# Kernel optimization log

Measured on AMD Instinct MI355X. Metric: run time of the kernel, lower is better.

The kernel has to match this reference:

```python
import jax, jax.numpy as jnp
import numpy as np

E = 1024      # hidden_size
H = 16        # num_attention_heads
HD = E // H   # head_dim
EPS = 1e-5


def _mw_linear(x, Wt, bt, Wi, bi, split):
    # multiway linear: text weights on tokens [:split], image weights on [split:]
    xt = x[:, :split] @ Wt.T + bt
    xi = x[:, split:] @ Wi.T + bi
    return jnp.concatenate([xt, xi], axis=1)


def _ln(x, g, b):
    mu = jnp.mean(x, axis=-1, keepdims=True)
    var = jnp.mean(jnp.square(x - mu), axis=-1, keepdims=True)
    return (x - mu) * jax.lax.rsqrt(var + EPS) * g + b


def _mw_ln(x, gt, bt, gi, bi, split):
    return jnp.concatenate([_ln(x[:, :split], gt, bt), _ln(x[:, split:], gi, bi)], axis=1)


def setup_inputs() -> dict:
    key = jax.random.key(0)
    ks = jax.random.split(key, 24)
    B, T = 8, 1024
    d = {
        'query': jax.random.normal(ks[0], (B, T, E), jnp.float32),
        'key': jax.random.normal(ks[1], (B, T, E), jnp.float32),
        'value': jax.random.normal(ks[2], (B, T, E), jnp.float32),
        'attention_mask': jax.random.normal(ks[3], (T, T), jnp.float32) * 0.02,
    }
    i = 4
    for name in ['q', 'k', 'v', 'o']:
        d[f'W{name}_t'] = jax.random.normal(ks[i], (E, E), jnp.float32) * 0.02; i += 1
        d[f'b{name}_t'] = jnp.zeros((E,), jnp.float32)
        d[f'W{name}_i'] = jax.random.normal(ks[i], (E, E), jnp.float32) * 0.02; i += 1
        d[f'b{name}_i'] = jnp.zeros((E,), jnp.float32)
    d['ln_g_t'] = jnp.ones((E,), jnp.float32)
    d['ln_b_t'] = jnp.zeros((E,), jnp.float32)
    d['ln_g_i'] = jnp.ones((E,), jnp.float32)
    d['ln_b_i'] = jnp.zeros((E,), jnp.float32)
    d['split_position'] = 64
    return d


def reference(query, key, value, attention_mask,
              Wq_t, bq_t, Wq_i, bq_i,
              Wk_t, bk_t, Wk_i, bk_i,
              Wv_t, bv_t, Wv_i, bv_i,
              Wo_t, bo_t, Wo_i, bo_i,
              ln_g_t, ln_b_t, ln_g_i, ln_b_i,
              split_position):
    B, T, _ = query.shape
    S = key.shape[1]
    scaling = HD ** -0.5
    q = _mw_linear(query, Wq_t, bq_t, Wq_i, bq_i, split_position) * scaling
    k = _mw_linear(key, Wk_t, bk_t, Wk_i, bk_i, split_position)
    v = _mw_linear(value, Wv_t, bv_t, Wv_i, bv_i, split_position)
    q = q.reshape(B, T, H, HD)
    k = k.reshape(B, S, H, HD)
    v = v.reshape(B, S, H, HD)
    # [B, H, T, S] attention logits
    attn_weights = jnp.einsum('bthd,bshd->bhts', q, k)
    attn_weights = jnp.nan_to_num(attn_weights) + attention_mask[None, None]
    probs = jax.nn.softmax(attn_weights.astype(jnp.float32), axis=-1).astype(attn_weights.dtype)
    attn = jnp.einsum('bhts,bshd->bthd', probs, v).reshape(B, T, E)
    attn = _mw_ln(attn, ln_g_t, ln_b_t, ln_g_i, ln_b_i, split_position)
    attn = _mw_linear(attn, Wo_t, bo_t, Wo_i, bo_i, split_position)
    return attn
```

## Files before the change

### kernel.cpp

```cpp
#include <hip/hip_runtime.h>

#define E_DIM 1024
#define HEADS 16
#define HD 64

typedef unsigned short ushort_t;
typedef __attribute__((ext_vector_type(8))) short bf16x8;
typedef __attribute__((ext_vector_type(4))) float floatx4;

__device__ inline unsigned int pack2bf(float a, float b) {
    unsigned int ua = __builtin_bit_cast(unsigned int, a);
    unsigned int ub = __builtin_bit_cast(unsigned int, b);
    ua = (ua + 0x8000u) >> 16;
    ub = (ub + 0x8000u) & 0xFFFF0000u;
    return ua | ub;
}
__device__ inline unsigned short f2bf(float a) {
    return (unsigned short)((__builtin_bit_cast(unsigned int, a) + 0x8000u) >> 16);
}
__device__ inline float bf2f(unsigned int s) {
    return __builtin_bit_cast(float, s << 16);
}

__device__ __forceinline__ void load_lds16(const void* g, void* l) {
    __builtin_amdgcn_global_load_lds(
        (const __attribute__((address_space(1))) unsigned int*)g,
        (__attribute__((address_space(3))) unsigned int*)l, 16, 0, 0);
}

__global__ __launch_bounds__(256) void cvt_inputs(
    const float* s0, const float* s1, const float* s2,
    ushort_t* d0, ushort_t* d1, ushort_t* d2)
{
    const float* __restrict__ src = (blockIdx.y == 0) ? s0 : (blockIdx.y == 1) ? s1 : s2;
    ushort_t* __restrict__ dst = (blockIdx.y == 0) ? d0 : (blockIdx.y == 1) ? d1 : d2;
    size_t i = ((size_t)blockIdx.x * 256 + threadIdx.x) * 8;
    float4 a = *(const float4*)&src[i];
    float4 b = *(const float4*)&src[i + 4];
    uint4 o;
    o.x = pack2bf(a.x, a.y); o.y = pack2bf(a.z, a.w);
    o.z = pack2bf(b.x, b.y); o.w = pack2bf(b.z, b.w);
    *(uint4*)&dst[i] = o;
}

__global__ __launch_bounds__(256) void cvt_weights(
    const float* w0, const float* w1, const float* w2, const float* w3,
    const float* w4, const float* w5, const float* w6, const float* w7,
    ushort_t* __restrict__ out)
{
    const float* srcs[8] = {w0, w1, w2, w3, w4, w5, w6, w7};
    const float* __restrict__ src = srcs[blockIdx.y];
    ushort_t* __restrict__ dst = out + (size_t)blockIdx.y * E_DIM * E_DIM;
    size_t i = ((size_t)blockIdx.x * 256 + threadIdx.x) * 8;
    float4 a = *(const float4*)&src[i];
    float4 b = *(const float4*)&src[i + 4];
    uint4 o;
    o.x = pack2bf(a.x, a.y); o.y = pack2bf(a.z, a.w);
    o.z = pack2bf(b.x, b.y); o.w = pack2bf(b.z, b.w);
    *(uint4*)&dst[i] = o;
}

template<bool OUT_BF16>
__device__ __forceinline__ void gemm_core(
    const ushort_t* __restrict__ x, const ushort_t* __restrict__ W,
    const float* __restrict__ bias, void* __restrict__ outv,
    int m0, int n0, int split, int kind, float scale, int T_)
{
    __shared__ __align__(16) ushort_t As[128 * 32];
    __shared__ __align__(16) ushort_t Bs[128 * 32];

    const int tid  = threadIdx.x;
    const int lane = tid & 63;
    const int wv   = tid >> 6;
    const int rw   = (wv >> 1) * 64;
    const int cw   = (wv & 1) * 64;
    const int am   = lane & 15;
    const int aq   = lane >> 4;

    const int grow = wv * 32 + (lane >> 2);
    const int gcol = (lane & 3) * 8;

    floatx4 acc[4][4];
    #pragma unroll
    for (int i = 0; i < 4; ++i)
        #pragma unroll
        for (int j = 0; j < 4; ++j)
            acc[i][j] = (floatx4){0.f, 0.f, 0.f, 0.f};

    for (int k0 = 0; k0 < E_DIM; k0 += 32) {
        load_lds16(&x[(size_t)(m0 + grow) * E_DIM + k0 + gcol],      &As[(wv * 32) * 32]);
        load_lds16(&x[(size_t)(m0 + grow + 16) * E_DIM + k0 + gcol], &As[(wv * 32 + 16) * 32]);
        load_lds16(&W[(size_t)(n0 + grow) * E_DIM + k0 + gcol],      &Bs[(wv * 32) * 32]);
        load_lds16(&W[(size_t)(n0 + grow + 16) * E_DIM + k0 + gcol], &Bs[(wv * 32 + 16) * 32]);
        __syncthreads();

        bf16x8 af[4], bfv[4];
        #pragma unroll
        for (int i = 0; i < 4; ++i)
            af[i] = *(const bf16x8*)&As[(rw + i * 16 + am) * 32 + aq * 8];
        #pragma unroll
        for (int j = 0; j < 4; ++j)
            bfv[j] = *(const bf16x8*)&Bs[(cw + j * 16 + am) * 32 + aq * 8];

        #pragma unroll
        for (int i = 0; i < 4; ++i)
            #pragma unroll
            for (int j = 0; j < 4; ++j)
                acc[i][j] = __builtin_amdgcn_mfma_f32_16x16x32_bf16(af[i], bfv[j], acc[i][j], 0, 0, 0);
        __syncthreads();
    }

    const int cq = lane >> 4;
    const int cm = lane & 15;
    #pragma unroll
    for (int j = 0; j < 4; ++j) {
        int n = n0 + cw + j * 16 + cm;
        float bv = bias[n];
        #pragma unroll
        for (int i = 0; i < 4; ++i) {
            int mbase = m0 + rw + i * 16 + cq * 4;
            #pragma unroll
            for (int r = 0; r < 4; ++r) {
                int m = mbase + r;
                int t = m % T_;
                if (((t < split) ? 0 : 1) != kind) continue;
                float val = (acc[i][j][r] + bv) * scale;
                if (OUT_BF16) ((ushort_t*)outv)[(size_t)m * E_DIM + n] = f2bf(val);
                else          ((float*)outv)[(size_t)m * E_DIM + n] = val;
            }
        }
    }
}

__global__ __launch_bounds__(256) void gemm_qkv(
    const ushort_t* __restrict__ xq, const ushort_t* __restrict__ xk,
    const ushort_t* __restrict__ xv, const ushort_t* __restrict__ wall,
    const float* bq_t, const float* bq_i, const float* bk_t, const float* bk_i,
    const float* bv_t, const float* bv_i,
    ushort_t* oq, ushort_t* ok, ushort_t* ov,
    const int* __restrict__ split_ptr, int T_)
{
    const int split = *split_ptr;
    const int z = blockIdx.z;
    const int op = z >> 1;
    const int kind = z & 1;
    const int m0 = blockIdx.y * 128;
    const int n0 = blockIdx.x * 128;
    const int t0 = m0 % T_;

    if (kind == 0) { if (t0 >= split) return; }
    else           { if (t0 + 128 <= split) return; }

    const ushort_t* x = (op == 0) ? xq : (op == 1) ? xk : xv;
    ushort_t* outp    = (op == 0) ? oq : (op == 1) ? ok : ov;
    const ushort_t* W = wall + (size_t)z * E_DIM * E_DIM;
    const float* bias = (op == 0) ? (kind ? bq_i : bq_t)
                      : (op == 1) ? (kind ? bk_i : bk_t)
                                  : (kind ? bv_i : bv_t);
    float scale = (op == 0) ? 0.125f : 1.0f;

    gemm_core<true>(x, W, bias, outp, m0, n0, split, kind, scale, T_);
}

__global__ __launch_bounds__(256) void gemm_o(
    const ushort_t* __restrict__ x, const ushort_t* __restrict__ Wt,
    const float* bt, const ushort_t* __restrict__ Wi, const float* bi,
    float* __restrict__ outp, const int* __restrict__ split_ptr, int T_)
{
    const int split = *split_ptr;
    const int kind = blockIdx.z;
    const int m0 = blockIdx.y * 128;
    const int n0 = blockIdx.x * 128;
    const int t0 = m0 % T_;

    if (kind == 0) { if (t0 >= split) return; }
    else           { if (t0 + 128 <= split) return; }

    gemm_core<false>(x, kind ? Wi : Wt, kind ? bi : bt, outp, m0, n0, split, kind, 1.0f, T_);
}

__global__ __launch_bounds__(256) void attn_mfma4(
    const ushort_t* __restrict__ q, const ushort_t* __restrict__ k,
    const ushort_t* __restrict__ v, const float* __restrict__ mask,
    ushort_t* __restrict__ outp, int T_)
{
    const int tid  = threadIdx.x;
    const int lane = tid & 63;
    const int wv   = tid >> 6;
    const int b    = blockIdx.x;
    const int h    = blockIdx.y;
    const int r0   = blockIdx.z * 128;

    __shared__ __align__(16) unsigned short Ks[5120];
    __shared__ __align__(16) unsigned short Vst[5120];
    __shared__ __align__(16) unsigned short Ps[4 * 1280];

    const int m    = lane & 15;
    const int kq   = lane >> 4;
    const int wrow = wv * 16;

    bf16x8 aq[2][2];
    #pragma unroll
    for (int qs = 0; qs < 2; ++qs)
        #pragma unroll
        for (int c = 0; c < 2; ++c)
            aq[qs][c] = *(const bf16x8*)&q[((size_t)(b * T_ + r0 + qs * 64 + wrow + m)) * E_DIM
                                           + h * HD + c * 32 + kq * 8];

    floatx4 oa[2][4];
    float mrun[2][4], lsum[2][4];
    #pragma unroll
    for (int qs = 0; qs < 2; ++qs)
        #pragma unroll
        for (int j = 0; j < 4; ++j) {
            oa[qs][j] = (floatx4){0.f, 0.f, 0.f, 0.f};
            mrun[qs][j] = -3.0e38f; lsum[qs][j] = 0.f;
        }

    const int krow = tid >> 4;
    const int kc4  = (tid & 15) * 4;
    const int kad  = (kc4 >> 5) * 2560 + krow * 40 + (kc4 & 31);
    const int vs0  = (tid >> 4) * 4;
    const int vd0  = (tid & 15) * 4;
    const int vplane = (vs0 >> 5) * 2560;
    const int vsin   = vs0 & 31;

    uint2 kreg[4], vreg[4];

    #pragma unroll
    for (int i = 0; i < 4; ++i)
        kreg[i] = *(const uint2*)&k[((size_t)(b * T_ + krow + 16 * i)) * E_DIM + h * HD + kc4];
    #pragma unroll
    for (int i = 0; i < 4; ++i)
        vreg[i] = *(const uint2*)&v[((size_t)(b * T_ + vs0 + i)) * E_DIM + h * HD + vd0];

    #pragma unroll
    for (int i = 0; i < 4; ++i) {
        int ad = kad + 16 * i * 40;
        *(unsigned int*)&Ks[ad]     = kreg[i].x;
        *(unsigned int*)&Ks[ad + 2] = kreg[i].y;
    }
    {
        const ushort_t* vp = (const ushort_t*)vreg;
        #pragma unroll
        for (int t = 0; t < 4; ++t) {
            int d  = vd0 + t;
            int pr = d ^ ((d >> 4) & 3);
            uint2 w;
            w.x = (unsigned int)vp[0 * 4 + t] | ((unsigned int)vp[1 * 4 + t] << 16);
            w.y = (unsigned int)vp[2 * 4 + t] | ((unsigned int)vp[3 * 4 + t] << 16);
            *(uint2*)&Vst[vplane + pr * 40 + vsin] = w;
        }
    }
    __syncthreads();

    const int NT = T_ / 64;
    #pragma unroll 1
    for (int it = 0; it < NT; ++it) {
        const int s0 = it * 64;

        if (it + 1 < NT) {
            int s0n = s0 + 64;
            #pragma unroll
            for (int i = 0; i < 4; ++i)
                kreg[i] = *(const uint2*)&k[((size_t)(b * T_ + s0n + krow + 16 * i)) * E_DIM + h * HD + kc4];
            #pragma unroll
            for (int i = 0; i < 4; ++i)
                vreg[i] = *(const uint2*)&v[((size_t)(b * T_ + s0n + vs0 + i)) * E_DIM + h * HD + vd0];
        }

        #pragma unroll
        for (int qs = 0; qs < 2; ++qs) {
            float mv[4][4];
            {
                const float* mbase = &mask[(size_t)(r0 + qs * 64 + wrow + kq * 4) * T_ + s0 + m];
                #pragma unroll
                for (int j = 0; j < 4; ++j)
                    #pragma unroll
                    for (int r = 0; r < 4; ++r)
                        mv[j][r] = mbase[r * T_ + j * 16];
            }

            floatx4 sa[4];
            #pragma unroll
            for (int j = 0; j < 4; ++j) sa[j] = (floatx4){0.f, 0.f, 0.f, 0.f};
            __builtin_amdgcn_s_setprio(1);
            #pragma unroll
            for (int c = 0; c < 2; ++c) {
                #pragma unroll
                for (int j = 0; j < 4; ++j) {
                    bf16x8 bk = *(const bf16x8*)&Ks[c * 2560 + (j * 16 + m) * 40 + kq * 8];
                    sa[j] = __builtin_amdgcn_mfma_f32_16x16x32_bf16(aq[qs][c], bk, sa[j], 0, 0, 0);
                }
            }
            __builtin_amdgcn_s_setprio(0);

            float mt[4];
            #pragma unroll
            for (int r = 0; r < 4; ++r) {
                sa[0][r] += mv[0][r]; sa[1][r] += mv[1][r];
                sa[2][r] += mv[2][r]; sa[3][r] += mv[3][r];
                float m2 = fmaxf(fmaxf(sa[0][r], sa[1][r]), fmaxf(sa[2][r], sa[3][r]));
                m2 = fmaxf(m2, __shfl_xor(m2, 1));
                m2 = fmaxf(m2, __shfl_xor(m2, 2));
                m2 = fmaxf(m2, __shfl_xor(m2, 4));
                m2 = fmaxf(m2, __shfl_xor(m2, 8));
                mt[r] = m2;
            }
            float need = fmaxf(fmaxf(mt[0] - mrun[qs][0], mt[1] - mrun[qs][1]),
                               fmaxf(mt[2] - mrun[qs][2], mt[3] - mrun[qs][3]));
            if (!__all(need <= 8.0f)) {
                #pragma unroll
                for (int r = 0; r < 4; ++r) {
                    float mn = fmaxf(mrun[qs][r], mt[r]);
                    float a  = __expf(mrun[qs][r] - mn);
                    mrun[qs][r] = mn;
                    lsum[qs][r] *= a;
                    #pragma unroll
                    for (int j = 0; j < 4; ++j)
                        oa[qs][j][r] *= a;
                }
            }

            float rs[4] = {0.f, 0.f, 0.f, 0.f};
            #pragma unroll
            for (int j = 0; j < 4; ++j) {
                int gl = ((((j & 1) << 1) | (m >> 3)) ^ kq) & 3;
                int pbase = wv * 1280 + (j >> 1) * 640 + (kq * 4) * 40 + gl * 8 + (m & 7);
                #pragma unroll
                for (int r = 0; r < 4; ++r) {
                    float p = __expf(sa[j][r] - mrun[qs][r]);
                    rs[r] += p;
                    Ps[pbase + r * 40] = f2bf(p);
                }
            }
            #pragma unroll
            for (int r = 0; r < 4; ++r) {
                float s = rs[r];
                s += __shfl_xor(s, 1); s += __shfl_xor(s, 2);
                s += __shfl_xor(s, 4); s += __shfl_xor(s, 8);
                lsum[qs][r] += s;
            }

            __builtin_amdgcn_s_setprio(1);
            #pragma unroll
            for (int c = 0; c < 2; ++c) {
                bf16x8 ap = *(const bf16x8*)&Ps[wv * 1280 + c * 640 + m * 40 + ((kq ^ (m >> 2)) & 3) * 8];
                #pragma unroll
                for (int j = 0; j < 4; ++j) {
                    int pr = 16 * j + (m ^ j);
                    bf16x8 bv = *(const bf16x8*)&Vst[c * 2560 + pr * 40 + kq * 8];
                    oa[qs][j] = __builtin_amdgcn_mfma_f32_16x16x32_bf16(ap, bv, oa[qs][j], 0, 0, 0);
                }
            }
            __builtin_amdgcn_s_setprio(0);
        }

        if (it + 1 < NT) {
            __syncthreads();
            #pragma unroll
            for (int i = 0; i < 4; ++i) {
                int ad = kad + 16 * i * 40;
                *(unsigned int*)&Ks[ad]     = kreg[i].x;
                *(unsigned int*)&Ks[ad + 2] = kreg[i].y;
            }
            const ushort_t* vp = (const ushort_t*)vreg;
            #pragma unroll
            for (int t = 0; t < 4; ++t) {
                int d  = vd0 + t;
                int pr = d ^ ((d >> 4) & 3);
                uint2 w;
                w.x = (unsigned int)vp[0 * 4 + t] | ((unsigned int)vp[1 * 4 + t] << 16);
                w.y = (unsigned int)vp[2 * 4 + t] | ((unsigned int)vp[3 * 4 + t] << 16);
                *(uint2*)&Vst[vplane + pr * 40 + vsin] = w;
            }
            __syncthreads();
        }
    }

    #pragma unroll
    for (int qs = 0; qs < 2; ++qs)
        #pragma unroll
        for (int r = 0; r < 4; ++r) {
            float inv = 1.0f / lsum[qs][r];
            size_t orow = ((size_t)(b * T_ + r0 + qs * 64 + wrow + kq * 4 + r)) * E_DIM + h * HD;
            #pragma unroll
            for (int j = 0; j < 4; ++j)
                outp[orow + j * 16 + m] = f2bf(oa[qs][j][r] * inv);
        }
}

__global__ __launch_bounds__(256) void mw_ln_bf16(
    const ushort_t* __restrict__ x,
    const float* __restrict__ gt, const float* __restrict__ bt,
    const float* __restrict__ gi, const float* __restrict__ bi,
    ushort_t* __restrict__ out,
    const int* __restrict__ split_ptr, int T_)
{
    const int split = *split_ptr;
    const int row = blockIdx.x;
    const int t = row % T_;
    const float* __restrict__ g  = (t < split) ? gt : gi;
    const float* __restrict__ bb = (t < split) ? bt : bi;

    const int tid = threadIdx.x;
    const int lane = tid & 63;
    const int wid = tid >> 6;

    __shared__ float red[8];

    uint2 xv = *(const uint2*)&x[(size_t)row * E_DIM + tid * 4];
    float f0 = bf2f(xv.x & 0xffffu), f1 = bf2f(xv.x >> 16);
    float f2 = bf2f(xv.y & 0xffffu), f3 = bf2f(xv.y >> 16);
    float s = f0 + f1 + f2 + f3;
    #pragma unroll
    for (int off = 1; off < 64; off <<= 1) s += __shfl_xor(s, off, 64);
    if (lane == 0) red[wid] = s;
    __syncthreads();
    float mu = (red[0] + red[1] + red[2] + red[3]) * (1.0f / E_DIM);

    float d0 = f0 - mu, d1 = f1 - mu, d2 = f2 - mu, d3 = f3 - mu;
    float s2 = d0*d0 + d1*d1 + d2*d2 + d3*d3;
    #pragma unroll
    for (int off = 1; off < 64; off <<= 1) s2 += __shfl_xor(s2, off, 64);
    if (lane == 0) red[4 + wid] = s2;
    __syncthreads();
    float var = (red[4] + red[5] + red[6] + red[7]) * (1.0f / E_DIM);
    float rstd = rsqrtf(var + 1e-5f);

    float4 gv = *(const float4*)&g[tid * 4];
    float4 bv = *(const float4*)&bb[tid * 4];
    uint2 ov;
    ov.x = pack2bf(d0 * rstd * gv.x + bv.x, d1 * rstd * gv.y + bv.y);
    ov.y = pack2bf(d2 * rstd * gv.z + bv.z, d3 * rstd * gv.w + bv.w);
    *(uint2*)&out[(size_t)row * E_DIM + tid * 4] = ov;
}

extern "C" void kernel_launch(void* const* d_in, const int* in_sizes, int n_in,
                              void* d_out, int out_size, void* d_ws, size_t ws_size,
                              hipStream_t stream) {
    const float* query = (const float*)d_in[0];
    const float* key   = (const float*)d_in[1];
    const float* value = (const float*)d_in[2];
    const float* mask  = (const float*)d_in[3];
    const float* Wq_t = (const float*)d_in[4];  const float* bq_t = (const float*)d_in[5];
    const float* Wq_i = (const float*)d_in[6];  const float* bq_i = (const float*)d_in[7];
    const float* Wk_t = (const float*)d_in[8];  const float* bk_t = (const float*)d_in[9];
    const float* Wk_i = (const float*)d_in[10]; const float* bk_i = (const float*)d_in[11];
    const float* Wv_t = (const float*)d_in[12]; const float* bv_t = (const float*)d_in[13];
    const float* Wv_i = (const float*)d_in[14]; const float* bv_i = (const float*)d_in[15];
    const float* Wo_t = (const float*)d_in[16]; const float* bo_t = (const float*)d_in[17];
    const float* Wo_i = (const float*)d_in[18]; const float* bo_i = (const float*)d_in[19];
    const float* ln_g_t = (const float*)d_in[20]; const float* ln_b_t = (const float*)d_in[21];
    const float* ln_g_i = (const float*)d_in[22]; const float* ln_b_i = (const float*)d_in[23];
    const int* split = (const int*)d_in[24];

    float* out = (float*)d_out;

    const int BT = in_sizes[0] / E_DIM;
    const int T_ = 1024;
    const int B  = BT / T_;

    ushort_t* ws = (ushort_t*)d_ws;
    const size_t nx = (size_t)BT * E_DIM;
    const size_t nw = (size_t)E_DIM * E_DIM;
    ushort_t* xq_bf = ws;
    ushort_t* xk_bf = ws + nx;
    ushort_t* xv_bf = ws + 2 * nx;
    ushort_t* k_bf  = ws + 3 * nx;
    ushort_t* v_bf  = ws + 4 * nx;
    ushort_t* w_bf  = ws + 5 * nx;
    ushort_t* q_bf  = (ushort_t*)d_out;

    dim3 blk(256);
    const int cvt_blocks = (int)(nx / 2048);
    const int wcvt_blocks = (int)(nw / 2048);

    cvt_weights<<<dim3(wcvt_blocks, 8), blk, 0, stream>>>(
        Wq_t, Wq_i, Wk_t, Wk_i, Wv_t, Wv_i, Wo_t, Wo_i, w_bf);
    cvt_inputs<<<dim3(cvt_blocks, 3), blk, 0, stream>>>(
        query, key, value, xq_bf, xk_bf, xv_bf);

    gemm_qkv<<<dim3(E_DIM / 128, BT / 128, 6), blk, 0, stream>>>(
        xq_bf, xk_bf, xv_bf, w_bf,
        bq_t, bq_i, bk_t, bk_i, bv_t, bv_i,
        q_bf, k_bf, v_bf, split, T_);

    attn_mfma4<<<dim3(B, HEADS, T_ / 128), blk, 0, stream>>>(
        q_bf, k_bf, v_bf, mask, q_bf, T_);

    mw_ln_bf16<<<dim3(BT), blk, 0, stream>>>(
        q_bf, ln_g_t, ln_b_t, ln_g_i, ln_b_i, xq_bf, split, T_);

    gemm_o<<<dim3(E_DIM / 128, BT / 128, 2), blk, 0, stream>>>(
        xq_bf, w_bf + 6 * nw, bo_t, w_bf + 7 * nw, bo_i, out, split, T_);
}
```

Before: 498.2 us.

## Share K/V LDS fragments across both query sub-tiles and defer row-sum reduction

Restructures the attention inner loop so the QK^T MFMAs for both 64-row query sub-tiles run together, each K fragment read from LDS once and reused for both. The PV stage likewise loads V fragments once and applies them to both sub-tiles, which needs a doubled P buffer in LDS. Per-row softmax sums are kept per-lane and shuffle-reduced only once at the end instead of every iteration. This cuts LDS reads and shuffles but raises register pressure (two score accumulators live) and LDS footprint, which could lower occupancy.

Result: faster. 478.9 us (-3.9%).

```diff
diff --git a/kernel.cpp b/kernel.cpp
--- a/kernel.cpp
+++ b/kernel.cpp
@@ -193,7 +193,7 @@
 
     __shared__ __align__(16) unsigned short Ks[5120];
     __shared__ __align__(16) unsigned short Vst[5120];
-    __shared__ __align__(16) unsigned short Ps[4 * 1280];
+    __shared__ __align__(16) unsigned short Ps[8 * 1280];
 
     const int m    = lane & 15;
     const int kq   = lane >> 4;
@@ -268,6 +268,26 @@
             for (int i = 0; i < 4; ++i)
                 vreg[i] = *(const uint2*)&v[((size_t)(b * T_ + s0n + vs0 + i)) * E_DIM + h * HD + vd0];
         }
+
+        floatx4 sa[2][4];
+        #pragma unroll
+        for (int qs = 0; qs < 2; ++qs)
+            #pragma unroll
+            for (int j = 0; j < 4; ++j) sa[qs][j] = (floatx4){0.f, 0.f, 0.f, 0.f};
+        __builtin_amdgcn_s_setprio(1);
+        #pragma unroll
+        for (int c = 0; c < 2; ++c) {
+            bf16x8 bkf[4];
+            #pragma unroll
+            for (int j = 0; j < 4; ++j)
+                bkf[j] = *(const bf16x8*)&Ks[c * 2560 + (j * 16 + m) * 40 + kq * 8];
+            #pragma unroll
+            for (int qs = 0; qs < 2; ++qs)
+                #pragma unroll
+                for (int j = 0; j < 4; ++j)
+                    sa[qs][j] = __builtin_amdgcn_mfma_f32_16x16x32_bf16(aq[qs][c], bkf[j], sa[qs][j], 0, 0, 0);
+        }
+        __builtin_amdgcn_s_setprio(0);
 
         #pragma unroll
         for (int qs = 0; qs < 2; ++qs) {
@@ -281,26 +301,13 @@
                         mv[j][r] = mbase[r * T_ + j * 16];
             }
 
-            floatx4 sa[4];
-            #pragma unroll
-            for (int j = 0; j < 4; ++j) sa[j] = (floatx4){0.f, 0.f, 0.f, 0.f};
-            __builtin_amdgcn_s_setprio(1);
-            #pragma unroll
-            for (int c = 0; c < 2; ++c) {
-                #pragma unroll
-                for (int j = 0; j < 4; ++j) {
-                    bf16x8 bk = *(const bf16x8*)&Ks[c * 2560 + (j * 16 + m) * 40 + kq * 8];
-                    sa[j] = __builtin_amdgcn_mfma_f32_16x16x32_bf16(aq[qs][c], bk, sa[j], 0, 0, 0);
-                }
-            }
-            __builtin_amdgcn_s_setprio(0);
-
             float mt[4];
             #pragma unroll
             for (int r = 0; r < 4; ++r) {
-                sa[0][r] += mv[0][r]; sa[1][r] += mv[1][r];
-                sa[2][r] += mv[2][r]; sa[3][r] += mv[3][r];
-                float m2 = fmaxf(fmaxf(sa[0][r], sa[1][r]), fmaxf(sa[2][r], sa[3][r]));
+                sa[qs][0][r] += mv[0][r]; sa[qs][1][r] += mv[1][r];
+                sa[qs][2][r] += mv[2][r]; sa[qs][3][r] += mv[3][r];
+                float m2 = fmaxf(fmaxf(sa[qs][0][r], sa[qs][1][r]),
+                                 fmaxf(sa[qs][2][r], sa[qs][3][r]));
                 m2 = fmaxf(m2, __shfl_xor(m2, 1));
                 m2 = fmaxf(m2, __shfl_xor(m2, 2));
                 m2 = fmaxf(m2, __shfl_xor(m2, 4));
@@ -322,39 +329,38 @@
                 }
             }
 
-            float rs[4] = {0.f, 0.f, 0.f, 0.f};
             #pragma unroll
             for (int j = 0; j < 4; ++j) {
                 int gl = ((((j & 1) << 1) | (m >> 3)) ^ kq) & 3;
-                int pbase = wv * 1280 + (j >> 1) * 640 + (kq * 4) * 40 + gl * 8 + (m & 7);
+                int pbase = (wv * 2 + qs) * 1280 + (j >> 1) * 640 + (kq * 4) * 40 + gl * 8 + (m & 7);
                 #pragma unroll
                 for (int r = 0; r < 4; ++r) {
-                    float p = __expf(sa[j][r] - mrun[qs][r]);
-                    rs[r] += p;
+                    float p = __expf(sa[qs][j][r] - mrun[qs][r]);
+                    lsum[qs][r] += p;
                     Ps[pbase + r * 40] = f2bf(p);
                 }
             }
-            #pragma unroll
-            for (int r = 0; r < 4; ++r) {
-                float s = rs[r];
-                s += __shfl_xor(s, 1); s += __shfl_xor(s, 2);
-                s += __shfl_xor(s, 4); s += __shfl_xor(s, 8);
-                lsum[qs][r] += s;
-            }
-
-            __builtin_amdgcn_s_setprio(1);
-            #pragma unroll
-            for (int c = 0; c < 2; ++c) {
-                bf16x8 ap = *(const bf16x8*)&Ps[wv * 1280 + c * 640 + m * 40 + ((kq ^ (m >> 2)) & 3) * 8];
+        }
+
+        __builtin_amdgcn_s_setprio(1);
+        #pragma unroll
+        for (int c = 0; c < 2; ++c) {
+            bf16x8 bvf[4];
+            #pragma unroll
+            for (int j = 0; j < 4; ++j) {
+                int pr = 16 * j + (m ^ j);
+                bvf[j] = *(const bf16x8*)&Vst[c * 2560 + pr * 40 + kq * 8];
+            }
+            #pragma unroll
+            for (int qs = 0; qs < 2; ++qs) {
+                bf16x8 ap = *(const bf16x8*)&Ps[(wv * 2 + qs) * 1280 + c * 640 + m * 40
+                                                + ((kq ^ (m >> 2)) & 3) * 8];
                 #pragma unroll
-                for (int j = 0; j < 4; ++j) {
-                    int pr = 16 * j + (m ^ j);
-                    bf16x8 bv = *(const bf16x8*)&Vst[c * 2560 + pr * 40 + kq * 8];
-                    oa[qs][j] = __builtin_amdgcn_mfma_f32_16x16x32_bf16(ap, bv, oa[qs][j], 0, 0, 0);
-                }
-            }
-            __builtin_amdgcn_s_setprio(0);
-        }
+                for (int j = 0; j < 4; ++j)
+                    oa[qs][j] = __builtin_amdgcn_mfma_f32_16x16x32_bf16(ap, bvf[j], oa[qs][j], 0, 0, 0);
+            }
+        }
+        __builtin_amdgcn_s_setprio(0);
 
         if (it + 1 < NT) {
             __syncthreads();
@@ -382,7 +388,10 @@
     for (int qs = 0; qs < 2; ++qs)
         #pragma unroll
         for (int r = 0; r < 4; ++r) {
-            float inv = 1.0f / lsum[qs][r];
+            float s = lsum[qs][r];
+            s += __shfl_xor(s, 1); s += __shfl_xor(s, 2);
+            s += __shfl_xor(s, 4); s += __shfl_xor(s, 8);
+            float inv = 1.0f / s;
             size_t orow = ((size_t)(b * T_ + r0 + qs * 64 + wrow + kq * 4 + r)) * E_DIM + h * HD;
             #pragma unroll
             for (int j = 0; j < 4; ++j)
```

## Rewrite attention with 32x32 MFMA, transposed S^T scores, and exp2 softmax

Applied to the files above, without the earlier changes.

The attention kernel moves from 16x16x32 MFMA tiles to 32x32x16 tiles and computes S^T = K·Q^T, so each lane owns one query row. The P fragments for the PV MFMA are then built in registers with cross-half shuffles instead of a round trip through LDS. The softmax switches to exp2 by folding log2e into the Q scale, and a new pre-pass kernel transposes and pre-scales the mask, written into a freed workspace buffer. The aim is fewer LDS round trips, fewer instructions per tile and cheaper exponentials. In exchange it adds an extra kernel launch, per-element shuffles for the rescale and output steps, and strided mask reads.

After: 488.7 us. About the same (-1.9%).

```diff
diff --git a/kernel.cpp b/kernel.cpp
--- a/kernel.cpp
+++ b/kernel.cpp
@@ -3,10 +3,12 @@
 #define E_DIM 1024
 #define HEADS 16
 #define HD 64
+#define LOG2E 1.44269504088896340736f
 
 typedef unsigned short ushort_t;
 typedef __attribute__((ext_vector_type(8))) short bf16x8;
 typedef __attribute__((ext_vector_type(4))) float floatx4;
+typedef __attribute__((ext_vector_type(16))) float floatx16;
 
 __device__ inline unsigned int pack2bf(float a, float b) {
     unsigned int ua = __builtin_bit_cast(unsigned int, a);
@@ -60,6 +62,32 @@
     *(uint4*)&dst[i] = o;
 }
 
+__global__ __launch_bounds__(256) void mask_tr(
+    const float* __restrict__ m, float* __restrict__ mt, int T_)
+{
+    __shared__ float tile[64][65];
+    const int bx = blockIdx.x * 64;
+    const int by = blockIdx.y * 64;
+    const int tc = (threadIdx.x & 15) * 4;
+    const int tr = threadIdx.x >> 4;
+    #pragma unroll
+    for (int rr = 0; rr < 64; rr += 16) {
+        float4 vv = *(const float4*)&m[(size_t)(by + tr + rr) * T_ + bx + tc];
+        tile[tr + rr][tc]     = vv.x; tile[tr + rr][tc + 1] = vv.y;
+        tile[tr + rr][tc + 2] = vv.z; tile[tr + rr][tc + 3] = vv.w;
+    }
+    __syncthreads();
+    #pragma unroll
+    for (int rr = 0; rr < 64; rr += 16) {
+        float4 ov;
+        ov.x = tile[tc + 0][tr + rr] * LOG2E;
+        ov.y = tile[tc + 1][tr + rr] * LOG2E;
+        ov.z = tile[tc + 2][tr + rr] * LOG2E;
+        ov.w = tile[tc + 3][tr + rr] * LOG2E;
+        *(float4*)&mt[(size_t)(bx + tr + rr) * T_ + by + tc] = ov;
+    }
+}
+
 template<bool OUT_BF16>
 __device__ __forceinline__ void gemm_core(
     const ushort_t* __restrict__ x, const ushort_t* __restrict__ W,
@@ -157,7 +185,7 @@
     const float* bias = (op == 0) ? (kind ? bq_i : bq_t)
                       : (op == 1) ? (kind ? bk_i : bk_t)
                                   : (kind ? bv_i : bv_t);
-    float scale = (op == 0) ? 0.125f : 1.0f;
+    float scale = (op == 0) ? 0.125f * LOG2E : 1.0f;
 
     gemm_core<true>(x, W, bias, outp, m0, n0, split, kind, scale, T_);
 }
@@ -179,9 +207,9 @@
     gemm_core<false>(x, kind ? Wi : Wt, kind ? bi : bt, outp, m0, n0, split, kind, 1.0f, T_);
 }
 
-__global__ __launch_bounds__(256) void attn_mfma4(
+__global__ __launch_bounds__(256) void attn_mfma32(
     const ushort_t* __restrict__ q, const ushort_t* __restrict__ k,
-    const ushort_t* __restrict__ v, const float* __restrict__ mask,
+    const ushort_t* __restrict__ v, const float* __restrict__ maskT,
     ushort_t* __restrict__ outp, int T_)
 {
     const int tid  = threadIdx.x;
@@ -191,65 +219,50 @@
     const int h    = blockIdx.y;
     const int r0   = blockIdx.z * 128;
 
-    __shared__ __align__(16) unsigned short Ks[5120];
-    __shared__ __align__(16) unsigned short Vst[5120];
-    __shared__ __align__(16) unsigned short Ps[4 * 1280];
-
-    const int m    = lane & 15;
-    const int kq   = lane >> 4;
-    const int wrow = wv * 16;
-
-    bf16x8 aq[2][2];
-    #pragma unroll
-    for (int qs = 0; qs < 2; ++qs)
-        #pragma unroll
-        for (int c = 0; c < 2; ++c)
-            aq[qs][c] = *(const bf16x8*)&q[((size_t)(b * T_ + r0 + qs * 64 + wrow + m)) * E_DIM
-                                           + h * HD + c * 32 + kq * 8];
-
-    floatx4 oa[2][4];
-    float mrun[2][4], lsum[2][4];
-    #pragma unroll
-    for (int qs = 0; qs < 2; ++qs)
-        #pragma unroll
-        for (int j = 0; j < 4; ++j) {
-            oa[qs][j] = (floatx4){0.f, 0.f, 0.f, 0.f};
-            mrun[qs][j] = -3.0e38f; lsum[qs][j] = 0.f;
-        }
-
-    const int krow = tid >> 4;
-    const int kc4  = (tid & 15) * 4;
-    const int kad  = (kc4 >> 5) * 2560 + krow * 40 + (kc4 & 31);
-    const int vs0  = (tid >> 4) * 4;
-    const int vd0  = (tid & 15) * 4;
-    const int vplane = (vs0 >> 5) * 2560;
-    const int vsin   = vs0 & 31;
-
-    uint2 kreg[4], vreg[4];
-
+    const int q32 = lane & 31;
+    const int hi  = lane >> 5;
+
+    __shared__ __align__(16) ushort_t Ks[64 * 72];
+    __shared__ __align__(16) ushort_t VT[64 * 72];
+
+    const int qrow = r0 + wv * 32 + q32;
+
+    bf16x8 aqf[4];
+    #pragma unroll
+    for (int dc = 0; dc < 4; ++dc)
+        aqf[dc] = *(const bf16x8*)&q[((size_t)(b * T_ + qrow)) * E_DIM + h * HD + dc * 16 + hi * 8];
+
+    floatx16 oa[2];
+    #pragma unroll
+    for (int n = 0; n < 2; ++n)
+        #pragma unroll
+        for (int i = 0; i < 16; ++i) oa[n][i] = 0.f;
+    float mrun = -1.0e30f, lsum = 0.f;
+
+    const int kr = tid >> 2;
+    const int kc = (tid & 3) * 16;
+    const int vr = (tid >> 4) * 4;
+    const int vc = (tid & 15) * 4;
+
+    uint4 kreg[2];
+    uint2 vreg[4];
+
+    kreg[0] = *(const uint4*)&k[((size_t)(b * T_ + kr)) * E_DIM + h * HD + kc];
+    kreg[1] = *(const uint4*)&k[((size_t)(b * T_ + kr)) * E_DIM + h * HD + kc + 8];
     #pragma unroll
     for (int i = 0; i < 4; ++i)
-        kreg[i] = *(const uint2*)&k[((size_t)(b * T_ + krow + 16 * i)) * E_DIM + h * HD + kc4];
-    #pragma unroll
-    for (int i = 0; i < 4; ++i)
-        vreg[i] = *(const uint2*)&v[((size_t)(b * T_ + vs0 + i)) * E_DIM + h * HD + vd0];
-
-    #pragma unroll
-    for (int i = 0; i < 4; ++i) {
-        int ad = kad + 16 * i * 40;
-        *(unsigned int*)&Ks[ad]     = kreg[i].x;
-        *(unsigned int*)&Ks[ad + 2] = kreg[i].y;
-    }
+        vreg[i] = *(const uint2*)&v[((size_t)(b * T_ + vr + i)) * E_DIM + h * HD + vc];
+
+    *(uint4*)&Ks[kr * 72 + kc]     = kreg[0];
+    *(uint4*)&Ks[kr * 72 + kc + 8] = kreg[1];
     {
         const ushort_t* vp = (const ushort_t*)vreg;
         #pragma unroll
         for (int t = 0; t < 4; ++t) {
-            int d  = vd0 + t;
-            int pr = d ^ ((d >> 4) & 3);
             uint2 w;
             w.x = (unsigned int)vp[0 * 4 + t] | ((unsigned int)vp[1 * 4 + t] << 16);
             w.y = (unsigned int)vp[2 * 4 + t] | ((unsigned int)vp[3 * 4 + t] << 16);
-            *(uint2*)&Vst[vplane + pr * 40 + vsin] = w;
+            *(uint2*)&VT[(vc + t) * 72 + vr] = w;
         }
     }
     __syncthreads();
@@ -260,134 +273,137 @@
         const int s0 = it * 64;
 
         if (it + 1 < NT) {
-            int s0n = s0 + 64;
+            const int sn = s0 + 64;
+            kreg[0] = *(const uint4*)&k[((size_t)(b * T_ + sn + kr)) * E_DIM + h * HD + kc];
+            kreg[1] = *(const uint4*)&k[((size_t)(b * T_ + sn + kr)) * E_DIM + h * HD + kc + 8];
             #pragma unroll
             for (int i = 0; i < 4; ++i)
-                kreg[i] = *(const uint2*)&k[((size_t)(b * T_ + s0n + krow + 16 * i)) * E_DIM + h * HD + kc4];
-            #pragma unroll
-            for (int i = 0; i < 4; ++i)
-                vreg[i] = *(const uint2*)&v[((size_t)(b * T_ + s0n + vs0 + i)) * E_DIM + h * HD + vd0];
+                vreg[i] = *(const uint2*)&v[((size_t)(b * T_ + sn + vr + i)) * E_DIM + h * HD + vc];
         }
 
-        #pragma unroll
-        for (int qs = 0; qs < 2; ++qs) {
-            float mv[4][4];
-            {
-                const float* mbase = &mask[(size_t)(r0 + qs * 64 + wrow + kq * 4) * T_ + s0 + m];
-                #pragma unroll
-                for (int j = 0; j < 4; ++j)
-                    #pragma unroll
-                    for (int r = 0; r < 4; ++r)
-                        mv[j][r] = mbase[r * T_ + j * 16];
-            }
-
-            floatx4 sa[4];
-            #pragma unroll
-            for (int j = 0; j < 4; ++j) sa[j] = (floatx4){0.f, 0.f, 0.f, 0.f};
-            __builtin_amdgcn_s_setprio(1);
-            #pragma unroll
-            for (int c = 0; c < 2; ++c) {
-                #pragma unroll
-                for (int j = 0; j < 4; ++j) {
-                    bf16x8 bk = *(const bf16x8*)&Ks[c * 2560 + (j * 16 + m) * 40 + kq * 8];
-                    sa[j] = __builtin_amdgcn_mfma_f32_16x16x32_bf16(aq[qs][c], bk, sa[j], 0, 0, 0);
-                }
-            }
-            __builtin_amdgcn_s_setprio(0);
-
-            float mt[4];
-            #pragma unroll
-            for (int r = 0; r < 4; ++r) {
-                sa[0][r] += mv[0][r]; sa[1][r] += mv[1][r];
-                sa[2][r] += mv[2][r]; sa[3][r] += mv[3][r];
-                float m2 = fmaxf(fmaxf(sa[0][r], sa[1][r]), fmaxf(sa[2][r], sa[3][r]));
-                m2 = fmaxf(m2, __shfl_xor(m2, 1));
-                m2 = fmaxf(m2, __shfl_xor(m2, 2));
-                m2 = fmaxf(m2, __shfl_xor(m2, 4));
-                m2 = fmaxf(m2, __shfl_xor(m2, 8));
-                mt[r] = m2;
-            }
-            float need = fmaxf(fmaxf(mt[0] - mrun[qs][0], mt[1] - mrun[qs][1]),
-                               fmaxf(mt[2] - mrun[qs][2], mt[3] - mrun[qs][3]));
-            if (!__all(need <= 8.0f)) {
-                #pragma unroll
-                for (int r = 0; r < 4; ++r) {
-                    float mn = fmaxf(mrun[qs][r], mt[r]);
-                    float a  = __expf(mrun[qs][r] - mn);
-                    mrun[qs][r] = mn;
-                    lsum[qs][r] *= a;
-                    #pragma unroll
-                    for (int j = 0; j < 4; ++j)
-                        oa[qs][j][r] *= a;
-                }
-            }
-
-            float rs[4] = {0.f, 0.f, 0.f, 0.f};
-            #pragma unroll
-            for (int j = 0; j < 4; ++j) {
-                int gl = ((((j & 1) << 1) | (m >> 3)) ^ kq) & 3;
-                int pbase = wv * 1280 + (j >> 1) * 640 + (kq * 4) * 40 + gl * 8 + (m & 7);
-                #pragma unroll
-                for (int r = 0; r < 4; ++r) {
-                    float p = __expf(sa[j][r] - mrun[qs][r]);
-                    rs[r] += p;
-                    Ps[pbase + r * 40] = f2bf(p);
-                }
-            }
-            #pragma unroll
-            for (int r = 0; r < 4; ++r) {
-                float s = rs[r];
-                s += __shfl_xor(s, 1); s += __shfl_xor(s, 2);
-                s += __shfl_xor(s, 4); s += __shfl_xor(s, 8);
-                lsum[qs][r] += s;
-            }
-
-            __builtin_amdgcn_s_setprio(1);
-            #pragma unroll
-            for (int c = 0; c < 2; ++c) {
-                bf16x8 ap = *(const bf16x8*)&Ps[wv * 1280 + c * 640 + m * 40 + ((kq ^ (m >> 2)) & 3) * 8];
-                #pragma unroll
-                for (int j = 0; j < 4; ++j) {
-                    int pr = 16 * j + (m ^ j);
-                    bf16x8 bv = *(const bf16x8*)&Vst[c * 2560 + pr * 40 + kq * 8];
-                    oa[qs][j] = __builtin_amdgcn_mfma_f32_16x16x32_bf16(ap, bv, oa[qs][j], 0, 0, 0);
-                }
-            }
-            __builtin_amdgcn_s_setprio(0);
+        float mv[2][16];
+        #pragma unroll
+        for (int j = 0; j < 2; ++j)
+            #pragma unroll
+            for (int i = 0; i < 16; ++i) {
+                int sr = s0 + 32 * j + (i & 3) + 8 * (i >> 2) + 4 * hi;
+                mv[j][i] = maskT[(size_t)sr * T_ + qrow];
+            }
+
+        floatx16 sa[2];
+        #pragma unroll
+        for (int j = 0; j < 2; ++j)
+            #pragma unroll
+            for (int i = 0; i < 16; ++i) sa[j][i] = 0.f;
+        __builtin_amdgcn_s_setprio(1);
+        #pragma unroll
+        for (int j = 0; j < 2; ++j)
+            #pragma unroll
+            for (int dc = 0; dc < 4; ++dc) {
+                bf16x8 kf = *(const bf16x8*)&Ks[(32 * j + q32) * 72 + dc * 16 + hi * 8];
+                sa[j] = __builtin_amdgcn_mfma_f32_32x32x16_bf16(kf, aqf[dc], sa[j], 0, 0, 0);
+            }
+        __builtin_amdgcn_s_setprio(0);
+
+        #pragma unroll
+        for (int j = 0; j < 2; ++j)
+            #pragma unroll
+            for (int i = 0; i < 16; ++i) sa[j][i] += mv[j][i];
+
+        float mx8[8];
+        #pragma unroll
+        for (int u = 0; u < 8; ++u)
+            mx8[u] = fmaxf(fmaxf(sa[0][2 * u], sa[0][2 * u + 1]),
+                           fmaxf(sa[1][2 * u], sa[1][2 * u + 1]));
+        float mt = fmaxf(fmaxf(fmaxf(mx8[0], mx8[1]), fmaxf(mx8[2], mx8[3])),
+                         fmaxf(fmaxf(mx8[4], mx8[5]), fmaxf(mx8[6], mx8[7])));
+        mt = fmaxf(mt, __shfl_xor(mt, 32, 64));
+
+        float need = mt - mrun;
+        if (!__all(need <= 11.0f)) {
+            float mn = fmaxf(mrun, mt);
+            float alpha = exp2f(mrun - mn);
+            mrun = mn;
+            lsum *= alpha;
+            #pragma unroll
+            for (int i = 0; i < 16; ++i) {
+                int qi = (i & 3) + 8 * (i >> 2) + 4 * hi;
+                float ai = __shfl(alpha, qi + (lane & 32), 64);
+                oa[0][i] *= ai;
+                oa[1][i] *= ai;
+            }
         }
+
+        float lp0 = 0.f, lp1 = 0.f, lp2 = 0.f, lp3 = 0.f;
+        #pragma unroll
+        for (int j = 0; j < 2; ++j)
+            #pragma unroll
+            for (int i = 0; i < 16; ++i) {
+                float e = exp2f(sa[j][i] - mrun);
+                sa[j][i] = e;
+                if ((i & 3) == 0) lp0 += e;
+                else if ((i & 3) == 1) lp1 += e;
+                else if ((i & 3) == 2) lp2 += e;
+                else lp3 += e;
+            }
+        lsum += (lp0 + lp1) + (lp2 + lp3);
+
+        unsigned int W[2][8], X[2][8];
+        #pragma unroll
+        for (int j = 0; j < 2; ++j)
+            #pragma unroll
+            for (int u = 0; u < 8; ++u)
+                W[j][u] = pack2bf(sa[j][2 * u], sa[j][2 * u + 1]);
+        #pragma unroll
+        for (int j = 0; j < 2; ++j)
+            #pragma unroll
+            for (int u = 0; u < 8; ++u)
+                X[j][u] = (unsigned int)__shfl_xor((int)W[j][u], 32, 64);
+
+        __builtin_amdgcn_s_setprio(1);
+        #pragma unroll
+        for (int s = 0; s < 4; ++s) {
+            const int j = s >> 1;
+            const int hh = (s & 1) * 4;
+            union { unsigned int u[4]; bf16x8 v8; } pf;
+            pf.u[0] = hi ? X[j][hh + 2] : W[j][hh + 0];
+            pf.u[1] = hi ? X[j][hh + 3] : W[j][hh + 1];
+            pf.u[2] = hi ? W[j][hh + 2] : X[j][hh + 0];
+            pf.u[3] = hi ? W[j][hh + 3] : X[j][hh + 1];
+            #pragma unroll
+            for (int n = 0; n < 2; ++n) {
+                bf16x8 vf = *(const bf16x8*)&VT[(n * 32 + q32) * 72 + s * 16 + hi * 8];
+                oa[n] = __builtin_amdgcn_mfma_f32_32x32x16_bf16(pf.v8, vf, oa[n], 0, 0, 0);
+            }
+        }
+        __builtin_amdgcn_s_setprio(0);
 
         if (it + 1 < NT) {
             __syncthreads();
-            #pragma unroll
-            for (int i = 0; i < 4; ++i) {
-                int ad = kad + 16 * i * 40;
-                *(unsigned int*)&Ks[ad]     = kreg[i].x;
-                *(unsigned int*)&Ks[ad + 2] = kreg[i].y;
-            }
+            *(uint4*)&Ks[kr * 72 + kc]     = kreg[0];
+            *(uint4*)&Ks[kr * 72 + kc + 8] = kreg[1];
             const ushort_t* vp = (const ushort_t*)vreg;
             #pragma unroll
             for (int t = 0; t < 4; ++t) {
-                int d  = vd0 + t;
-                int pr = d ^ ((d >> 4) & 3);
                 uint2 w;
                 w.x = (unsigned int)vp[0 * 4 + t] | ((unsigned int)vp[1 * 4 + t] << 16);
                 w.y = (unsigned int)vp[2 * 4 + t] | ((unsigned int)vp[3 * 4 + t] << 16);
-                *(uint2*)&Vst[vplane + pr * 40 + vsin] = w;
+                *(uint2*)&VT[(vc + t) * 72 + vr] = w;
             }
             __syncthreads();
         }
     }
 
-    #pragma unroll
-    for (int qs = 0; qs < 2; ++qs)
-        #pragma unroll
-        for (int r = 0; r < 4; ++r) {
-            float inv = 1.0f / lsum[qs][r];
-            size_t orow = ((size_t)(b * T_ + r0 + qs * 64 + wrow + kq * 4 + r)) * E_DIM + h * HD;
-            #pragma unroll
-            for (int j = 0; j < 4; ++j)
-                outp[orow + j * 16 + m] = f2bf(oa[qs][j][r] * inv);
-        }
+    lsum += __shfl_xor(lsum, 32, 64);
+    float inv = 1.0f / lsum;
+    #pragma unroll
+    for (int i = 0; i < 16; ++i) {
+        int qi = (i & 3) + 8 * (i >> 2) + 4 * hi;
+        float vi = __shfl(inv, qi + (lane & 32), 64);
+        size_t orow = ((size_t)(b * T_ + r0 + wv * 32 + qi)) * E_DIM + h * HD;
+        outp[orow + q32]      = f2bf(oa[0][i] * vi);
+        outp[orow + 32 + q32] = f2bf(oa[1][i] * vi);
+    }
 }
 
 __global__ __launch_bounds__(256) void mw_ln_bf16(
@@ -471,6 +487,7 @@
     ushort_t* v_bf  = ws + 4 * nx;
     ushort_t* w_bf  = ws + 5 * nx;
     ushort_t* q_bf  = (ushort_t*)d_out;
+    float* maskT    = (float*)xk_bf;
 
     dim3 blk(256);
     const int cvt_blocks = (int)(nx / 2048);
@@ -486,8 +503,10 @@
         bq_t, bq_i, bk_t, bk_i, bv_t, bv_i,
         q_bf, k_bf, v_bf, split, T_);
 
-    attn_mfma4<<<dim3(B, HEADS, T_ / 128), blk, 0, stream>>>(
-        q_bf, k_bf, v_bf, mask, q_bf, T_);
+    mask_tr<<<dim3(T_ / 64, T_ / 64), blk, 0, stream>>>(mask, maskT, T_);
+
+    attn_mfma32<<<dim3(B, HEADS, T_ / 128), blk, 0, stream>>>(
+        q_bf, k_bf, v_bf, maskT, q_bf, T_);
 
     mw_ln_bf16<<<dim3(BT), blk, 0, stream>>>(
         q_bf, ln_g_t, ln_b_t, ln_g_i, ln_b_i, xq_bf, split, T_);
```
